# Performance work log

Measured on AMD Instinct MI355X. Metric: run time of the kernel, lower is better.

Reference implementation:

```python
import jax, jax.numpy as jnp
import numpy as np

DRIVEWAY_CLASS = 1
FOOTPATH_CLASS = 2
CONF_THRESH = 0.3


def setup_inputs() -> dict:
    key = jax.random.key(0)
    k1, k2, k3 = jax.random.split(key, 3)
    B, N, C, H, W = 32, 300, 3, 1024, 1024
    det_boxes = jax.random.uniform(k1, (B, N, 4), dtype=jnp.float32)       # cxcywh in [0,1]
    det_confidence = jax.random.uniform(k2, (B, N), dtype=jnp.float32)
    seg_masks = jax.random.uniform(k3, (B, C, H, W), dtype=jnp.float32)
    return {"det_boxes": det_boxes, "det_confidence": det_confidence, "seg_masks": seg_masks}


def _box_sums(prob, y1, x1, y2, x2):
    """Sum of prob[b, y1:y2, x1:x2] for every (b, n) box via integral image.

    prob: (B, H, W); y1/x1/y2/x2: (B, N) int32. Returns (B, N)."""
    # zero-padded 2D prefix sum -> (B, H+1, W+1)
    ii = jnp.pad(jnp.cumsum(jnp.cumsum(prob, axis=1), axis=2), ((0, 0), (1, 0), (1, 0)))
    gather = jax.vmap(lambda ib, yy, xx: ib[yy, xx])  # per-batch fancy gather
    return gather(ii, y2, x2) - gather(ii, y1, x2) - gather(ii, y2, x1) + gather(ii, y1, x1)


def reference(det_boxes, det_confidence, seg_masks):
    B, N, _ = det_boxes.shape
    H, W = seg_masks.shape[2], seg_masks.shape[3]
    cx, cy, w, h = det_boxes[..., 0], det_boxes[..., 1], det_boxes[..., 2], det_boxes[..., 3]
    # cxcywh -> xyxy, scale to pixels; .long() truncates toward zero, then clamp to [0, dim-1]
    def to_idx(v, m):
        return jnp.clip(jnp.trunc(v).astype(jnp.int32), 0, m - 1)
    x1 = to_idx((cx - w / 2) * W, W)
    x2 = to_idx((cx + w / 2) * W, W)
    y1 = to_idx((cy - h / 2) * H, H)
    y2 = to_idx((cy + h / 2) * H, H)

    valid = (det_confidence >= CONF_THRESH) & (x2 > x1) & (y2 > y1)
    area = ((y2 - y1) * (x2 - x1)).astype(seg_masks.dtype)
    safe_area = jnp.where(area > 0, area, jnp.ones_like(area))

    dsum = _box_sums(seg_masks[:, DRIVEWAY_CLASS], y1, x1, y2, x2)  # (B, N)
    fsum = _box_sums(seg_masks[:, FOOTPATH_CLASS], y1, x1, y2, x2)  # (B, N)

    per_box = jax.nn.relu((fsum - dsum) / safe_area) * det_confidence
    total = jnp.sum(jnp.where(valid, per_box, jnp.zeros_like(per_box)))
    return total / max(B * N, 1)
```

## Files before the change

### kernel.cpp

```cpp
#include <hip/hip_runtime.h>

#define BB 32
#define NN 300
#define HH 1024
#define WW 1024
#define SEGR 64
#define NSEG 16

__global__ __launch_bounds__(256) void integral_kernel(
    const float* __restrict__ seg, float* __restrict__ I, size_t ibstride,
    float* __restrict__ segT)
{
    int blk  = blockIdx.x;
    int b    = blk >> 4;
    int s    = blk & 15;
    int t    = threadIdx.x;
    int lane = t & 63;
    int warp = t >> 6;
    int c0   = t * 4;
    int row0 = s * SEGR;

    const float* p1 = seg + ((size_t)b * 3 + 1) * ((size_t)HH * WW);
    const float* p2 = seg + ((size_t)b * 3 + 2) * ((size_t)HH * WW);
    float* Ib = I + (size_t)b * ibstride;

    __shared__ float wsum[2][4];

    float acc0 = 0.f, acc1 = 0.f, acc2 = 0.f, acc3 = 0.f;

    float4 f1 = *(const float4*)(p1 + (size_t)row0 * WW + c0);
    float4 f2 = *(const float4*)(p2 + (size_t)row0 * WW + c0);

    for (int y = 0; y < SEGR; ++y) {
        int row = row0 + y;
        float4 cf1 = f1, cf2 = f2;
        if (y + 1 < SEGR) {
            f1 = *(const float4*)(p1 + (size_t)(row + 1) * WW + c0);
            f2 = *(const float4*)(p2 + (size_t)(row + 1) * WW + c0);
        }
        float d0 = cf2.x - cf1.x;
        float d1 = cf2.y - cf1.y;
        float d2 = cf2.z - cf1.z;
        float d3 = cf2.w - cf1.w;
        float l1 = d0 + d1;
        float l2 = l1 + d2;
        float l3 = l2 + d3;

        float incl = l3;
        #pragma unroll
        for (int d = 1; d < 64; d <<= 1) {
            float v = __shfl_up(incl, d, 64);
            if (lane >= d) incl += v;
        }
        int p = y & 1;
        if (lane == 63) wsum[p][warp] = incl;
        __syncthreads();
        float base = incl - l3;
        #pragma unroll
        for (int w = 0; w < 3; ++w)
            if (warp > w) base += wsum[p][w];

        acc0 += base + d0;
        acc1 += base + l1;
        acc2 += base + l2;
        acc3 += base + l3;

        *(float4*)(Ib + (size_t)row * WW + c0) =
            make_float4(acc0, acc1, acc2, acc3);
    }
    *(float4*)(segT + (size_t)(b * NSEG + s) * WW + c0) =
        make_float4(acc0, acc1, acc2, acc3);
}

__global__ __launch_bounds__(256) void segscan_kernel(
    const float* __restrict__ segT, float* __restrict__ offs)
{
    int idx = blockIdx.x * blockDim.x + threadIdx.x;
    int b = idx >> 10;
    int x = idx & 1023;
    float run = 0.f;
    #pragma unroll
    for (int s = 0; s < NSEG; ++s) {
        size_t o = (size_t)(b * NSEG + s) * WW + x;
        float v = segT[o];
        offs[o] = run;
        run += v;
    }
}

__global__ __launch_bounds__(256) void gather_kernel(
    const float4* __restrict__ boxes, const float* __restrict__ conf,
    const float* __restrict__ I, size_t ibstride,
    const float* __restrict__ offs, float* __restrict__ out)
{
    int gid = blockIdx.x * blockDim.x + threadIdx.x;
    float local = 0.f;
    if (gid < BB * NN) {
        int b = gid / NN;
        float4 box = boxes[gid];
        float c = conf[gid];
        float cx = box.x, cy = box.y, w = box.z, h = box.w;
        float x1f = (cx - 0.5f * w) * (float)WW;
        float x2f = (cx + 0.5f * w) * (float)WW;
        float y1f = (cy - 0.5f * h) * (float)HH;
        float y2f = (cy + 0.5f * h) * (float)HH;
        int x1 = min(max((int)truncf(x1f), 0), WW - 1);
        int x2 = min(max((int)truncf(x2f), 0), WW - 1);
        int y1 = min(max((int)truncf(y1f), 0), HH - 1);
        int y2 = min(max((int)truncf(y2f), 0), HH - 1);
        bool valid = (c >= 0.3f) && (x2 > x1) && (y2 > y1);
        if (valid) {
            const float* Ib = I + (size_t)b * ibstride;
            const float* Ob = offs + (size_t)b * (NSEG * WW);
            auto corner = [&](int y, int x) -> float {
                if (y == 0 || x == 0) return 0.f;
                int yy = y - 1, xx = x - 1;
                return Ib[(size_t)yy * WW + xx] + Ob[(yy >> 6) * WW + xx];
            };
            float sum = corner(y2, x2) - corner(y1, x2)
                      - corner(y2, x1) + corner(y1, x1);
            float area = (float)((y2 - y1) * (x2 - x1));
            local = fmaxf(sum / area, 0.f) * c;
        }
    }
    #pragma unroll
    for (int d = 32; d > 0; d >>= 1)
        local += __shfl_down(local, d, 64);
    __shared__ float blksum[4];
    int lane = threadIdx.x & 63, warp = threadIdx.x >> 6;
    if (lane == 0) blksum[warp] = local;
    __syncthreads();
    if (threadIdx.x == 0) {
        float t = blksum[0] + blksum[1] + blksum[2] + blksum[3];
        atomicAdd(out, t * (1.0f / (BB * NN)));
    }
}

extern "C" void kernel_launch(void* const* d_in, const int* in_sizes, int n_in,
                              void* d_out, int out_size, void* d_ws, size_t ws_size,
                              hipStream_t stream) {
    const float* boxes = (const float*)d_in[0];
    const float* conf  = (const float*)d_in[1];
    const float* seg   = (const float*)d_in[2];
    float* out = (float*)d_out;

    const size_t i_bytes   = (size_t)BB * HH * WW * sizeof(float);
    const size_t aux_elems = (size_t)BB * NSEG * WW;
    const size_t aux_bytes = aux_elems * sizeof(float);

    float* I;
    size_t ibstride;
    float* segT;
    float* offs;
    if (ws_size >= i_bytes + 2 * aux_bytes) {
        I        = (float*)d_ws;
        ibstride = (size_t)HH * WW;
        segT     = (float*)((char*)d_ws + i_bytes);
        offs     = segT + aux_elems;
    } else {
        I        = (float*)d_in[2];
        ibstride = (size_t)3 * HH * WW;
        segT     = (float*)d_ws;
        offs     = segT + aux_elems;
    }

    hipMemsetAsync(d_out, 0, sizeof(float), stream);
    integral_kernel<<<BB * NSEG, 256, 0, stream>>>(seg, I, ibstride, segT);
    segscan_kernel<<<(BB * WW) / 256, 256, 0, stream>>>(segT, offs);
    gather_kernel<<<(BB * NN + 255) / 256, 256, 0, stream>>>(
        (const float4*)boxes, conf, I, ibstride, offs, out);
}
```

Measured before the change: 529.9 us.

## Replace full integral image with per-strip row prefix sums and box accumulation

Drops the full 2D integral image that was written to global memory. Each block now computes row-wise prefix sums of (footpath - driveway) for an 8-row strip in shared memory, and every box overlapping the strip adds its row-range sums into a per-box global accumulator with atomics. A single-block finalize kernel then applies area, relu and confidence and writes the mean. This removes the large integral-image write, the segment scan pass and the scattered gathers. In exchange it adds per-strip box loops (all 300 boxes checked in each of the 4096 blocks) and global atomics, and changes the floating-point summation order.

```diff
diff --git a/kernel.cpp b/kernel.cpp
--- a/kernel.cpp
+++ b/kernel.cpp
@@ -4,169 +4,150 @@
 #define NN 300
 #define HH 1024
 #define WW 1024
-#define SEGR 64
-#define NSEG 16
+#define RSTRIP 8
+#define NSTRIP (HH / RSTRIP)
 
-__global__ __launch_bounds__(256) void integral_kernel(
-    const float* __restrict__ seg, float* __restrict__ I, size_t ibstride,
-    float* __restrict__ segT)
+__global__ __launch_bounds__(256) void strip_kernel(
+    const float* __restrict__ seg,
+    const float4* __restrict__ boxes,
+    const float* __restrict__ conf,
+    float* __restrict__ boxacc)
 {
     int blk  = blockIdx.x;
-    int b    = blk >> 4;
-    int s    = blk & 15;
+    int b    = blk >> 7;
+    int s    = blk & (NSTRIP - 1);
+    int r0   = s * RSTRIP;
     int t    = threadIdx.x;
     int lane = t & 63;
     int warp = t >> 6;
-    int c0   = t * 4;
-    int row0 = s * SEGR;
+
+    __shared__ float L[RSTRIP][WW];
 
     const float* p1 = seg + ((size_t)b * 3 + 1) * ((size_t)HH * WW);
     const float* p2 = seg + ((size_t)b * 3 + 2) * ((size_t)HH * WW);
-    float* Ib = I + (size_t)b * ibstride;
 
-    __shared__ float wsum[2][4];
+    int row0 = r0 + warp;
+    int row1 = r0 + 4 + warp;
+    const float* q1a = p1 + (size_t)row0 * WW + lane * 16;
+    const float* q2a = p2 + (size_t)row0 * WW + lane * 16;
+    const float* q1b = p1 + (size_t)row1 * WW + lane * 16;
+    const float* q2b = p2 + (size_t)row1 * WW + lane * 16;
 
-    float acc0 = 0.f, acc1 = 0.f, acc2 = 0.f, acc3 = 0.f;
+    float4 a0 = *(const float4*)(q1a +  0), a1 = *(const float4*)(q1a +  4);
+    float4 a2 = *(const float4*)(q1a +  8), a3 = *(const float4*)(q1a + 12);
+    float4 c0 = *(const float4*)(q2a +  0), c1 = *(const float4*)(q2a +  4);
+    float4 c2 = *(const float4*)(q2a +  8), c3 = *(const float4*)(q2a + 12);
+    float4 d0 = *(const float4*)(q1b +  0), d1 = *(const float4*)(q1b +  4);
+    float4 d2 = *(const float4*)(q1b +  8), d3 = *(const float4*)(q1b + 12);
+    float4 e0 = *(const float4*)(q2b +  0), e1 = *(const float4*)(q2b +  4);
+    float4 e2 = *(const float4*)(q2b +  8), e3 = *(const float4*)(q2b + 12);
 
-    float4 f1 = *(const float4*)(p1 + (size_t)row0 * WW + c0);
-    float4 f2 = *(const float4*)(p2 + (size_t)row0 * WW + c0);
-
-    for (int y = 0; y < SEGR; ++y) {
-        int row = row0 + y;
-        float4 cf1 = f1, cf2 = f2;
-        if (y + 1 < SEGR) {
-            f1 = *(const float4*)(p1 + (size_t)(row + 1) * WW + c0);
-            f2 = *(const float4*)(p2 + (size_t)(row + 1) * WW + c0);
+    #pragma unroll
+    for (int rr = 0; rr < 2; ++rr) {
+        float g[16];
+        if (rr == 0) {
+            g[ 0]=c0.x-a0.x; g[ 1]=c0.y-a0.y; g[ 2]=c0.z-a0.z; g[ 3]=c0.w-a0.w;
+            g[ 4]=c1.x-a1.x; g[ 5]=c1.y-a1.y; g[ 6]=c1.z-a1.z; g[ 7]=c1.w-a1.w;
+            g[ 8]=c2.x-a2.x; g[ 9]=c2.y-a2.y; g[10]=c2.z-a2.z; g[11]=c2.w-a2.w;
+            g[12]=c3.x-a3.x; g[13]=c3.y-a3.y; g[14]=c3.z-a3.z; g[15]=c3.w-a3.w;
+        } else {
+            g[ 0]=e0.x-d0.x; g[ 1]=e0.y-d0.y; g[ 2]=e0.z-d0.z; g[ 3]=e0.w-d0.w;
+            g[ 4]=e1.x-d1.x; g[ 5]=e1.y-d1.y; g[ 6]=e1.z-d1.z; g[ 7]=e1.w-d1.w;
+            g[ 8]=e2.x-d2.x; g[ 9]=e2.y-d2.y; g[10]=e2.z-d2.z; g[11]=e2.w-d2.w;
+            g[12]=e3.x-d3.x; g[13]=e3.y-d3.y; g[14]=e3.z-d3.z; g[15]=e3.w-d3.w;
         }
-        float d0 = cf2.x - cf1.x;
-        float d1 = cf2.y - cf1.y;
-        float d2 = cf2.z - cf1.z;
-        float d3 = cf2.w - cf1.w;
-        float l1 = d0 + d1;
-        float l2 = l1 + d2;
-        float l3 = l2 + d3;
-
-        float incl = l3;
+        float run = 0.f;
+        #pragma unroll
+        for (int j = 0; j < 16; ++j) { run += g[j]; g[j] = run; }
+        float incl = run;
         #pragma unroll
         for (int d = 1; d < 64; d <<= 1) {
             float v = __shfl_up(incl, d, 64);
             if (lane >= d) incl += v;
         }
-        int p = y & 1;
-        if (lane == 63) wsum[p][warp] = incl;
-        __syncthreads();
-        float base = incl - l3;
-        #pragma unroll
-        for (int w = 0; w < 3; ++w)
-            if (warp > w) base += wsum[p][w];
+        float base = incl - run;
+        int r = (rr == 0 ? warp : 4 + warp);
+        float* Lr = &L[r][lane * 16];
+        *(float4*)(Lr +  0) = make_float4(g[ 0]+base, g[ 1]+base, g[ 2]+base, g[ 3]+base);
+        *(float4*)(Lr +  4) = make_float4(g[ 4]+base, g[ 5]+base, g[ 6]+base, g[ 7]+base);
+        *(float4*)(Lr +  8) = make_float4(g[ 8]+base, g[ 9]+base, g[10]+base, g[11]+base);
+        *(float4*)(Lr + 12) = make_float4(g[12]+base, g[13]+base, g[14]+base, g[15]+base);
+    }
+    __syncthreads();
 
-        acc0 += base + d0;
-        acc1 += base + l1;
-        acc2 += base + l2;
-        acc3 += base + l3;
-
-        *(float4*)(Ib + (size_t)row * WW + c0) =
-            make_float4(acc0, acc1, acc2, acc3);
-    }
-    *(float4*)(segT + (size_t)(b * NSEG + s) * WW + c0) =
-        make_float4(acc0, acc1, acc2, acc3);
-}
-
-__global__ __launch_bounds__(256) void segscan_kernel(
-    const float* __restrict__ segT, float* __restrict__ offs)
-{
-    int idx = blockIdx.x * blockDim.x + threadIdx.x;
-    int b = idx >> 10;
-    int x = idx & 1023;
-    float run = 0.f;
-    #pragma unroll
-    for (int s = 0; s < NSEG; ++s) {
-        size_t o = (size_t)(b * NSEG + s) * WW + x;
-        float v = segT[o];
-        offs[o] = run;
-        run += v;
-    }
-}
-
-__global__ __launch_bounds__(256) void gather_kernel(
-    const float4* __restrict__ boxes, const float* __restrict__ conf,
-    const float* __restrict__ I, size_t ibstride,
-    const float* __restrict__ offs, float* __restrict__ out)
-{
-    int gid = blockIdx.x * blockDim.x + threadIdx.x;
-    float local = 0.f;
-    if (gid < BB * NN) {
-        int b = gid / NN;
-        float4 box = boxes[gid];
-        float c = conf[gid];
-        float cx = box.x, cy = box.y, w = box.z, h = box.w;
-        float x1f = (cx - 0.5f * w) * (float)WW;
-        float x2f = (cx + 0.5f * w) * (float)WW;
-        float y1f = (cy - 0.5f * h) * (float)HH;
-        float y2f = (cy + 0.5f * h) * (float)HH;
+    for (int n = t; n < NN; n += 256) {
+        int gi = b * NN + n;
+        float4 bx = boxes[gi];
+        float cf  = conf[gi];
+        float x1f = (bx.x - 0.5f * bx.z) * (float)WW;
+        float x2f = (bx.x + 0.5f * bx.z) * (float)WW;
+        float y1f = (bx.y - 0.5f * bx.w) * (float)HH;
+        float y2f = (bx.y + 0.5f * bx.w) * (float)HH;
         int x1 = min(max((int)truncf(x1f), 0), WW - 1);
         int x2 = min(max((int)truncf(x2f), 0), WW - 1);
         int y1 = min(max((int)truncf(y1f), 0), HH - 1);
         int y2 = min(max((int)truncf(y2f), 0), HH - 1);
-        bool valid = (c >= 0.3f) && (x2 > x1) && (y2 > y1);
-        if (valid) {
-            const float* Ib = I + (size_t)b * ibstride;
-            const float* Ob = offs + (size_t)b * (NSEG * WW);
-            auto corner = [&](int y, int x) -> float {
-                if (y == 0 || x == 0) return 0.f;
-                int yy = y - 1, xx = x - 1;
-                return Ib[(size_t)yy * WW + xx] + Ob[(yy >> 6) * WW + xx];
-            };
-            float sum = corner(y2, x2) - corner(y1, x2)
-                      - corner(y2, x1) + corner(y1, x1);
+        if (!((cf >= 0.3f) && (x2 > x1) && (y2 > y1))) continue;
+        int lo = max(y1, r0);
+        int hi = min(y2 - 1, r0 + RSTRIP - 1);
+        if (lo > hi) continue;
+        int xa = x2 - 1;
+        int xb = x1 - 1;
+        float sum = 0.f;
+        for (int r = lo; r <= hi; ++r) {
+            float v = L[r - r0][xa];
+            if (xb >= 0) v -= L[r - r0][xb];
+            sum += v;
+        }
+        atomicAdd(&boxacc[gi], sum);
+    }
+}
+
+__global__ __launch_bounds__(256) void finalize_kernel(
+    const float4* __restrict__ boxes,
+    const float* __restrict__ conf,
+    const float* __restrict__ boxacc,
+    float* __restrict__ out)
+{
+    int t = threadIdx.x;
+    float local = 0.f;
+    for (int i = t; i < BB * NN; i += 256) {
+        float4 bx = boxes[i];
+        float cf  = conf[i];
+        float x1f = (bx.x - 0.5f * bx.z) * (float)WW;
+        float x2f = (bx.x + 0.5f * bx.z) * (float)WW;
+        float y1f = (bx.y - 0.5f * bx.w) * (float)HH;
+        float y2f = (bx.y + 0.5f * bx.w) * (float)HH;
+        int x1 = min(max((int)truncf(x1f), 0), WW - 1);
+        int x2 = min(max((int)truncf(x2f), 0), WW - 1);
+        int y1 = min(max((int)truncf(y1f), 0), HH - 1);
+        int y2 = min(max((int)truncf(y2f), 0), HH - 1);
+        if ((cf >= 0.3f) && (x2 > x1) && (y2 > y1)) {
             float area = (float)((y2 - y1) * (x2 - x1));
-            local = fmaxf(sum / area, 0.f) * c;
+            local += fmaxf(boxacc[i] / area, 0.f) * cf;
         }
     }
     #pragma unroll
     for (int d = 32; d > 0; d >>= 1)
         local += __shfl_down(local, d, 64);
-    __shared__ float blksum[4];
-    int lane = threadIdx.x & 63, warp = threadIdx.x >> 6;
-    if (lane == 0) blksum[warp] = local;
+    __shared__ float bsum[4];
+    int lane = t & 63, warp = t >> 6;
+    if (lane == 0) bsum[warp] = local;
     __syncthreads();
-    if (threadIdx.x == 0) {
-        float t = blksum[0] + blksum[1] + blksum[2] + blksum[3];
-        atomicAdd(out, t * (1.0f / (BB * NN)));
-    }
+    if (t == 0)
+        out[0] = (bsum[0] + bsum[1] + bsum[2] + bsum[3]) * (1.0f / (BB * NN));
 }
 
 extern "C" void kernel_launch(void* const* d_in, const int* in_sizes, int n_in,
                               void* d_out, int out_size, void* d_ws, size_t ws_size,
                               hipStream_t stream) {
-    const float* boxes = (const float*)d_in[0];
-    const float* conf  = (const float*)d_in[1];
-    const float* seg   = (const float*)d_in[2];
-    float* out = (float*)d_out;
+    const float4* boxes = (const float4*)d_in[0];
+    const float*  conf  = (const float*)d_in[1];
+    const float*  seg   = (const float*)d_in[2];
+    float* out    = (float*)d_out;
+    float* boxacc = (float*)d_ws;
 
-    const size_t i_bytes   = (size_t)BB * HH * WW * sizeof(float);
-    const size_t aux_elems = (size_t)BB * NSEG * WW;
-    const size_t aux_bytes = aux_elems * sizeof(float);
-
-    float* I;
-    size_t ibstride;
-    float* segT;
-    float* offs;
-    if (ws_size >= i_bytes + 2 * aux_bytes) {
-        I        = (float*)d_ws;
-        ibstride = (size_t)HH * WW;
-        segT     = (float*)((char*)d_ws + i_bytes);
-        offs     = segT + aux_elems;
-    } else {
-        I        = (float*)d_in[2];
-        ibstride = (size_t)3 * HH * WW;
-        segT     = (float*)d_ws;
-        offs     = segT + aux_elems;
-    }
-
-    hipMemsetAsync(d_out, 0, sizeof(float), stream);
-    integral_kernel<<<BB * NSEG, 256, 0, stream>>>(seg, I, ibstride, segT);
-    segscan_kernel<<<(BB * WW) / 256, 256, 0, stream>>>(segT, offs);
-    gather_kernel<<<(BB * NN + 255) / 256, 256, 0, stream>>>(
-        (const float4*)boxes, conf, I, ibstride, offs, out);
+    hipMemsetAsync(boxacc, 0, (size_t)BB * NN * sizeof(float), stream);
+    strip_kernel<<<BB * NSTRIP, 256, 0, stream>>>(seg, boxes, conf, boxacc);
+    finalize_kernel<<<1, 256, 0, stream>>>(boxes, conf, boxacc, out);
 }
```

New measurement: 516.0 us. 1.03x faster.
